# Performance work log

Hardware: AMD Instinct MI355X
Metric: run time of the kernel (lower is better)

The kernel has to match this reference:

```python
import jax, jax.numpy as jnp
import numpy as np

N = 100000   # nodes
E = 1600000  # edges
D_IN, D_H, D_OUT = 128, 128, 64
BN_EPS = 1e-5


def setup_inputs() -> dict:
    key = jax.random.key(0)
    ks = jax.random.split(key, 12)

    def lin_w(k, fan_in, shape):
        s = 1.0 / np.sqrt(fan_in)
        return jax.random.uniform(k, shape, jnp.float32, -s, s)

    return {
        "x": jax.random.normal(ks[0], (N, D_IN), jnp.float32),
        "edge_index": jax.random.randint(ks[1], (2, E), 0, N, dtype=jnp.int64),
        "edge_weight": jax.random.uniform(ks[2], (E,), jnp.float32),
        "W1": lin_w(ks[3], D_IN, (D_IN, D_H)),
        "b1": jnp.zeros((D_H,), jnp.float32),
        "W2": lin_w(ks[4], D_H, (D_H, D_H)),
        "b2": jnp.zeros((D_H,), jnp.float32),
        "W3": lin_w(ks[5], D_H, (D_H, D_OUT)),
        "b3": jnp.zeros((D_OUT,), jnp.float32),
        "gamma1": jnp.ones((D_H,), jnp.float32),
        "beta1": jnp.zeros((D_H,), jnp.float32),
        "gamma2": jnp.ones((D_H,), jnp.float32),
        "beta2": jnp.zeros((D_H,), jnp.float32),
    }


def _gcn_conv(x, src, dst, w, W, b):
    # PyG GCNConv: x' = D^{-1/2} (A + I) D^{-1/2} (x W) + b, self-loop weight 1
    n = x.shape[0]
    h = x @ W                                   # [N, d_out]
    loop = jnp.arange(n, dtype=src.dtype)
    s = jnp.concatenate([src, loop])            # [E+N]
    d = jnp.concatenate([dst, loop])
    ww = jnp.concatenate([w, jnp.ones((n,), w.dtype)])
    deg = jax.ops.segment_sum(ww, d, num_segments=n)          # in-degree at targets
    dinv = jnp.where(deg > 0, jax.lax.rsqrt(deg), 0.0)
    norm = dinv[s] * ww * dinv[d]               # [E+N]
    msg = h[s] * norm[:, None]                  # gather + scale
    out = jax.ops.segment_sum(msg, d, num_segments=n)
    return out + b


def _batch_norm(x, gamma, beta):
    mean = jnp.mean(x, axis=0)
    var = jnp.mean(jnp.square(x - mean), axis=0)  # biased, as BatchNorm uses
    return (x - mean) * jax.lax.rsqrt(var + BN_EPS) * gamma + beta


def reference(x, edge_index, edge_weight, W1, b1, W2, b2, W3, b3,
              gamma1, beta1, gamma2, beta2):
    src, dst = edge_index[0], edge_index[1]
    h = _gcn_conv(x, src, dst, edge_weight, W1, b1)
    h = jax.nn.relu(_batch_norm(h, gamma1, beta1))
    h = _gcn_conv(h, src, dst, edge_weight, W2, b2)
    h = jax.nn.relu(_batch_norm(h, gamma2, beta2))
    return _gcn_conv(h, src, dst, edge_weight, W3, b3)
```

## Files before the change

kernel.cpp:

```cpp
#include <hip/hip_runtime.h>
#include <hip/hip_fp16.h>
#include <cstdint>
#include <cstddef>

#define BN_EPS 1e-5f
#define KB 1024
#define BSH 9

typedef _Float16 half8 __attribute__((ext_vector_type(8)));
typedef float floatx4 __attribute__((ext_vector_type(4)));

__device__ __forceinline__ float loadS(const __half* p) { return __half2float(*p); }
__device__ __forceinline__ float2 load2(const __half* p) {
    return __half22float2(*(const __half2*)p);
}
__device__ __forceinline__ void storeS(float* p, float v) { *p = v; }
__device__ __forceinline__ void storeS(__half* p, float v) { *p = __float2half(v); }
__device__ __forceinline__ void store2(float* p, float a, float b) {
    *(float2*)p = make_float2(a, b);
}
__device__ __forceinline__ void store2(__half* p, float a, float b) {
    *(__half2*)p = __floats2half2_rn(a, b);
}
__device__ __forceinline__ float wn_of(unsigned v) {
    __half_raw hr; hr.x = (unsigned short)(v & 0x7fffu);
    return __half2float((__half)hr);
}

static __device__ __forceinline__ int load_edge(const void* ei, int mode64, long long pos) {
    if (mode64) return (int)((const long long*)ei)[pos];
    return ((const int*)ei)[pos];
}

__device__ __forceinline__ int detect_mode64(const unsigned* eiw) {
    const int lane = (int)threadIdx.x & 63;
    unsigned m = 0;
    for (int i = lane; i < 2048; i += 64) m |= eiw[2 * i + 1];
    return (__ballot(m != 0) == 0ULL) ? 1 : 0;
}

__global__ __launch_bounds__(256) void init_hist_kernel(const void* __restrict__ ei,
                                                        unsigned* __restrict__ tk,
                                                        unsigned* __restrict__ pc, int E, int epb,
                                                        const float* __restrict__ W1,
                                                        const float* __restrict__ W2,
                                                        const float* __restrict__ W3,
                                                        _Float16* __restrict__ WT1,
                                                        _Float16* __restrict__ WT2,
                                                        _Float16* __restrict__ WT3) {
    const int bid = (int)blockIdx.x;
    const int tid = (int)threadIdx.x;
    if (bid < 160) {
        if (bid == 0 && tid < 8) tk[tid] = 0u;
        const int t_ = bid;
        if (t_ < 64) {
            int t = t_ * 256 + tid;
            int n = t / 128, k = t % 128;
            WT1[t] = (_Float16)W1[k * 128 + n];
        } else if (t_ < 128) {
            int t = (t_ - 64) * 256 + tid;
            int n = t / 128, k = t % 128;
            WT2[t] = (_Float16)W2[k * 128 + n];
        } else {
            int t = (t_ - 128) * 256 + tid;
            int n = t / 128, k = t % 128;
            WT3[t] = (_Float16)W3[k * 64 + n];
        }
        return;
    }
    __shared__ unsigned h[256];
    const int k = bid - 160;
    h[tid] = 0;
    __syncthreads();
    const int md = detect_mode64((const unsigned*)ei);
    const int e0 = k * epb;
    const int e1 = min(E, e0 + epb);
    for (int e = e0 + tid; e < e1; e += 256) {
        int d = load_edge(ei, md, (long long)E + e);
        atomicAdd(&h[d >> BSH], 1u);
    }
    __syncthreads();
    pc[k * 256 + tid] = h[tid];
}

__global__ __launch_bounds__(256) void scan_pc_kernel(unsigned* __restrict__ pc,
                                                      int* __restrict__ tb,
                                                      int* __restrict__ bbase,
                                                      float* __restrict__ gsum,
                                                      float* __restrict__ gsq,
                                                      unsigned* __restrict__ tk, int nbuck) {
    __shared__ int red[256];
    __shared__ int lastFlag;
    const int b = (int)blockIdx.x;
    const int tid = (int)threadIdx.x;
    unsigned v[4];
    int vals[4];
    int s = 0;
#pragma unroll
    for (int j = 0; j < 4; ++j) {
        v[j] = pc[(tid * 4 + j) * 256 + b];
        vals[j] = s;
        s += (int)v[j];
    }
    red[tid] = s;
    __syncthreads();
    for (int off = 1; off < 256; off <<= 1) {
        int t = 0;
        if (tid >= off) t = red[tid - off];
        __syncthreads();
        red[tid] += t;
        __syncthreads();
    }
    const int excl = red[tid] - s;
#pragma unroll
    for (int j = 0; j < 4; ++j)
        pc[(tid * 4 + j) * 256 + b] = (unsigned)(excl + vals[j]);
    if (tid == 255)
        __hip_atomic_store(&tb[b], red[255], __ATOMIC_RELEASE, __HIP_MEMORY_SCOPE_AGENT);
    __syncthreads();
    if (tid == 0) {
        unsigned t = __hip_atomic_fetch_add(tk, 1u, __ATOMIC_ACQ_REL, __HIP_MEMORY_SCOPE_AGENT);
        lastFlag = (t == (unsigned)gridDim.x - 1u) ? 1 : 0;
    }
    __syncthreads();
    if (!lastFlag) return;
    const int v2 = (tid < nbuck)
        ? __hip_atomic_load(&tb[tid], __ATOMIC_ACQUIRE, __HIP_MEMORY_SCOPE_AGENT) : 0;
    __syncthreads();
    red[tid] = v2;
    __syncthreads();
    for (int off = 1; off < 256; off <<= 1) {
        int t = 0;
        if (tid >= off) t = red[tid - off];
        __syncthreads();
        red[tid] += t;
        __syncthreads();
    }
    bbase[tid] = red[tid] - v2;
    if (tid < 128) { gsum[tid] = 0.0f; gsq[tid] = 0.0f; }
}

template <int M, bool BN, typename TI>
__device__ __forceinline__ void gemm_body(int gbid, const TI* __restrict__ X,
                                          const _Float16* __restrict__ WTg,
                                          const float* __restrict__ sc,
                                          const float* __restrict__ sh,
                                          __half* __restrict__ Hout, int N,
                                          _Float16* WT ) {
    constexpr int CT = M / 16;
    constexpr int LDK = 136;

    for (int t = threadIdx.x; t < M * 16; t += 256) {
        int n = t / 16, seg = t % 16;
        *(half8*)&WT[n * LDK + seg * 8] = *(const half8*)&WTg[n * 128 + seg * 8];
    }
    __syncthreads();

    const int wave = (int)threadIdx.x >> 6;
    const int lane = (int)threadIdx.x & 63;
    const int qd = lane >> 4;
    const int ln = lane & 15;
    const int tile0 = gbid * 64 + wave * 16;
    int ar = tile0 + ln;
    if (ar >= N) ar = N - 1;

    half8 aF[4];
    const TI* xr = X + (size_t)ar * 128 + qd * 8;
#pragma unroll
    for (int kb = 0; kb < 4; ++kb) {
        float vv[8];
        if constexpr (sizeof(TI) == 4) {
            float4 v0 = *(const float4*)(xr + kb * 32);
            float4 v1 = *(const float4*)(xr + kb * 32 + 4);
            vv[0] = v0.x; vv[1] = v0.y; vv[2] = v0.z; vv[3] = v0.w;
            vv[4] = v1.x; vv[5] = v1.y; vv[6] = v1.z; vv[7] = v1.w;
        } else {
            half8 raw = *(const half8*)(xr + kb * 32);
#pragma unroll
            for (int j = 0; j < 8; ++j) vv[j] = (float)raw[j];
        }
        if (BN) {
            const int kbase = kb * 32 + qd * 8;
#pragma unroll
            for (int j = 0; j < 8; ++j)
                vv[j] = fmaxf(fmaf(vv[j], sc[kbase + j], sh[kbase + j]), 0.0f);
        }
        half8 a;
#pragma unroll
        for (int j = 0; j < 8; ++j) a[j] = (_Float16)vv[j];
        aF[kb] = a;
    }

#pragma unroll
    for (int ct = 0; ct < CT; ++ct) {
        floatx4 acc = {0.0f, 0.0f, 0.0f, 0.0f};
#pragma unroll
        for (int kb = 0; kb < 4; ++kb) {
            half8 b = *(const half8*)&WT[(ct * 16 + ln) * LDK + kb * 32 + qd * 8];
            acc = __builtin_amdgcn_mfma_f32_16x16x32_f16(aF[kb], b, acc, 0, 0, 0);
        }
#pragma unroll
        for (int r = 0; r < 4; ++r) {
            int orow = tile0 + qd * 4 + r;
            if (orow < N) Hout[(size_t)orow * M + ct * 16 + ln] = __float2half(acc[r]);
        }
    }
}

__global__ __launch_bounds__(256) void sort_gemm1_kernel(const void* __restrict__ ei,
                                                         const float* __restrict__ ew,
                                                         const unsigned* __restrict__ pc,
                                                         const int* __restrict__ bbase,
                                                         unsigned long long* __restrict__ sortedE,
                                                         int E, int epb,
                                                         const float* __restrict__ X,
                                                         const _Float16* __restrict__ WT1g,
                                                         __half* __restrict__ Hout, int N) {
    __shared__ _Float16 WT[128 * 136];
    __shared__ unsigned off_s[256];
    if ((int)blockIdx.x >= KB) {
        gemm_body<128, false, float>((int)blockIdx.x - KB, X, WT1g, nullptr, nullptr,
                                     Hout, N, WT);
        return;
    }
    const int k = (int)blockIdx.x;
    const int tid = (int)threadIdx.x;
    off_s[tid] = (unsigned)bbase[tid] + pc[k * 256 + tid];
    __syncthreads();
    const int md = detect_mode64((const unsigned*)ei);
    const int e0 = k * epb;
    const int e1 = min(E, e0 + epb);
    for (int e = e0 + tid; e < e1; e += 256) {
        int d = load_edge(ei, md, (long long)E + e);
        int s = load_edge(ei, md, e);
        float wv = ew[e];
        unsigned slot = atomicAdd(&off_s[d >> BSH], 1u);
        sortedE[slot] = ((unsigned long long)(unsigned)d << 33) |
                        ((unsigned long long)(unsigned)s << 16) |
                        (unsigned long long)(unsigned short)__half_as_ushort(__float2half(wv));
    }
}

__global__ __launch_bounds__(256) void csr_build_kernel(const unsigned long long* __restrict__ sortedE,
                                                        const int* __restrict__ bbase,
                                                        const int* __restrict__ tb,
                                                        float* __restrict__ dinv,
                                                        int* __restrict__ cnt,
                                                        int* __restrict__ row_start,
                                                        unsigned* __restrict__ edata, int N) {
    __shared__ unsigned cs[512];
    __shared__ float ws[512];
    __shared__ float dv[512];
    __shared__ unsigned sc[512];
    __shared__ unsigned cur[512];
    __shared__ int red[256];
    const int b = (int)blockIdx.x;
    const int tid = (int)threadIdx.x;
    const int n0 = b << BSH;
    const int base = bbase[b];
    const int len = tb[b];

    cs[tid] = 0; cs[tid + 256] = 0;
    ws[tid] = 0.0f; ws[tid + 256] = 0.0f;
    cur[tid] = 0; cur[tid + 256] = 0;
    __syncthreads();

    for (int i = tid; i < len; i += 256) {
        unsigned long long p = sortedE[base + i];
        unsigned fine = (unsigned)(p >> 33) - (unsigned)n0;
        atomicAdd(&cs[fine], 1u);
        __half_raw hr; hr.x = (unsigned short)(p & 0xFFFFu);
        atomicAdd(&ws[fine], __half2float((__half)hr));
    }
    __syncthreads();

    const unsigned a0 = cs[2 * tid];
    const unsigned a1 = cs[2 * tid + 1];
    const int s2 = (int)(a0 + a1);
    red[tid] = s2;
    __syncthreads();
    for (int off = 1; off < 256; off <<= 1) {
        int t = 0;
        if (tid >= off) t = red[tid - off];
        __syncthreads();
        red[tid] += t;
        __syncthreads();
    }
    const int excl2 = red[tid] - s2;
    sc[2 * tid] = (unsigned)excl2;
    sc[2 * tid + 1] = (unsigned)(excl2 + (int)a0);

#pragma unroll
    for (int q = 0; q < 2; ++q) {
        const int f = tid + q * 256;
        const int node = n0 + f;
        const float dvv = rsqrtf(1.0f + ws[f]);
        dv[f] = dvv;
        if (node < N) {
            dinv[node] = dvv;
            cnt[node] = (int)cs[f];
            row_start[node] = base + (int)sc[f];
        }
    }
    __syncthreads();

    for (int i = tid; i < len; i += 256) {
        unsigned long long p = sortedE[base + i];
        unsigned fine = (unsigned)(p >> 33) - (unsigned)n0;
        unsigned s = (unsigned)(p >> 16) & 0x1FFFFu;
        __half_raw hr; hr.x = (unsigned short)(p & 0xFFFFu);
        float wnp = __half2float((__half)hr) * dv[fine];
        unsigned r = atomicAdd(&cur[fine], 1u);
        unsigned hb = (unsigned)__half_as_ushort(__float2half(wnp)) & 0x7fffu;
        edata[base + (int)sc[fine] + (int)r] = (s << 15) | hb;
    }
}

template <int D, bool BIAS, typename TY>
__global__ __launch_bounds__(256) void agg_kernel(const __half* __restrict__ H,
                                                  const unsigned* __restrict__ edata,
                                                  const int* __restrict__ row_start,
                                                  const int* __restrict__ cnt,
                                                  const float* __restrict__ dinv,
                                                  const float* __restrict__ bias,
                                                  TY* __restrict__ Y, int N) {
    constexpr int VPT = D / 64;
    const int lane = (int)threadIdx.x & 63;
    const int i = (int)blockIdx.x * 4 + ((int)threadIdx.x >> 6);
    if (i >= N) return;
    const int c0 = lane * VPT;
    const float di = dinv[i];
    const float dii = di * di;

    float acc0, acc1 = 0.0f;
    if constexpr (VPT == 2) {
        float2 h = load2(H + (size_t)i * D + c0);
        acc0 = dii * h.x;
        acc1 = dii * h.y;
    } else {
        acc0 = dii * loadS(H + (size_t)i * D + c0);
    }

    const int base = row_start[i];
    const int n = cnt[i];
    for (int off = 0; off < n; off += 64) {
        const int rem = n - off;
        unsigned ev = 0;
        if (lane < rem) ev = edata[base + off + lane];
        const int mm = min(64, rem);
        for (int j = 0; j < mm; j += 8) {
            const unsigned e0 = __shfl(ev, j),     e1 = __shfl(ev, j + 1);
            const unsigned e2 = __shfl(ev, j + 2), e3 = __shfl(ev, j + 3);
            const unsigned e4 = __shfl(ev, j + 4), e5 = __shfl(ev, j + 5);
            const unsigned e6 = __shfl(ev, j + 6), e7 = __shfl(ev, j + 7);
            const float w0 = dinv[e0 >> 15] * wn_of(e0);
            const float w1 = dinv[e1 >> 15] * wn_of(e1);
            const float w2 = dinv[e2 >> 15] * wn_of(e2);
            const float w3 = dinv[e3 >> 15] * wn_of(e3);
            const float w4 = dinv[e4 >> 15] * wn_of(e4);
            const float w5 = dinv[e5 >> 15] * wn_of(e5);
            const float w6 = dinv[e6 >> 15] * wn_of(e6);
            const float w7 = dinv[e7 >> 15] * wn_of(e7);
            if constexpr (VPT == 2) {
                float2 h0 = load2(H + (size_t)(e0 >> 15) * D + c0);
                float2 h1 = load2(H + (size_t)(e1 >> 15) * D + c0);
                float2 h2 = load2(H + (size_t)(e2 >> 15) * D + c0);
                float2 h3 = load2(H + (size_t)(e3 >> 15) * D + c0);
                float2 h4 = load2(H + (size_t)(e4 >> 15) * D + c0);
                float2 h5 = load2(H + (size_t)(e5 >> 15) * D + c0);
                float2 h6 = load2(H + (size_t)(e6 >> 15) * D + c0);
                float2 h7 = load2(H + (size_t)(e7 >> 15) * D + c0);
                acc0 = fmaf(w0, h0.x, acc0); acc1 = fmaf(w0, h0.y, acc1);
                acc0 = fmaf(w1, h1.x, acc0); acc1 = fmaf(w1, h1.y, acc1);
                acc0 = fmaf(w2, h2.x, acc0); acc1 = fmaf(w2, h2.y, acc1);
                acc0 = fmaf(w3, h3.x, acc0); acc1 = fmaf(w3, h3.y, acc1);
                acc0 = fmaf(w4, h4.x, acc0); acc1 = fmaf(w4, h4.y, acc1);
                acc0 = fmaf(w5, h5.x, acc0); acc1 = fmaf(w5, h5.y, acc1);
                acc0 = fmaf(w6, h6.x, acc0); acc1 = fmaf(w6, h6.y, acc1);
                acc0 = fmaf(w7, h7.x, acc0); acc1 = fmaf(w7, h7.y, acc1);
            } else {
                float h0 = loadS(H + (size_t)(e0 >> 15) * D + c0);
                float h1 = loadS(H + (size_t)(e1 >> 15) * D + c0);
                float h2 = loadS(H + (size_t)(e2 >> 15) * D + c0);
                float h3 = loadS(H + (size_t)(e3 >> 15) * D + c0);
                float h4 = loadS(H + (size_t)(e4 >> 15) * D + c0);
                float h5 = loadS(H + (size_t)(e5 >> 15) * D + c0);
                float h6 = loadS(H + (size_t)(e6 >> 15) * D + c0);
                float h7 = loadS(H + (size_t)(e7 >> 15) * D + c0);
                acc0 = fmaf(w0, h0, acc0);
                acc0 = fmaf(w1, h1, acc0);
                acc0 = fmaf(w2, h2, acc0);
                acc0 = fmaf(w3, h3, acc0);
                acc0 = fmaf(w4, h4, acc0);
                acc0 = fmaf(w5, h5, acc0);
                acc0 = fmaf(w6, h6, acc0);
                acc0 = fmaf(w7, h7, acc0);
            }
        }
    }

    if constexpr (VPT == 2) {
        if (BIAS) { acc0 += bias[c0]; acc1 += bias[c0 + 1]; }
        store2(Y + (size_t)i * D + c0, acc0, acc1);
    } else {
        if (BIAS) acc0 += bias[c0];
        storeS(Y + (size_t)i * D + c0, acc0);
    }
}

template <int M, bool BN, typename TI, bool ZERO>
__global__ __launch_bounds__(256) void gemm_mfma_kernel(const TI* __restrict__ X,
                                                        const _Float16* __restrict__ WTg,
                                                        const float* __restrict__ sc,
                                                        const float* __restrict__ sh,
                                                        __half* __restrict__ Hout, int N,
                                                        float* __restrict__ gsum,
                                                        float* __restrict__ gsq, int GB) {
    __shared__ _Float16 WT[M * 136];
    if (ZERO && (int)blockIdx.x == GB) {
        if (threadIdx.x < 128) { gsum[threadIdx.x] = 0.0f; gsq[threadIdx.x] = 0.0f; }
        return;
    }
    gemm_body<M, BN, TI>(blockIdx.x, X, WTg, sc, sh, Hout, N, WT);
}

__global__ __launch_bounds__(256) void stats_kernel(const __half* __restrict__ Y,
                                                    float* __restrict__ gsum,
                                                    float* __restrict__ gsq,
                                                    unsigned* __restrict__ tk,
                                                    const float* __restrict__ gamma,
                                                    const float* __restrict__ beta,
                                                    float* __restrict__ sc,
                                                    float* __restrict__ sh, int N) {
    __shared__ float ls[256], lq[256];
    __shared__ int lastFlag;
    const int tid = (int)threadIdx.x;
    const int c = tid & 127;
    const int half_ = tid >> 7;
    float s = 0.0f, q = 0.0f;
    for (int row = (int)blockIdx.x * 2 + half_; row < N; row += 512) {
        float v = __half2float(Y[(size_t)row * 128 + c]);
        s += v;
        q = fmaf(v, v, q);
    }
    ls[tid] = s; lq[tid] = q;
    __syncthreads();
    if (tid < 128) {
        atomicAdd(&gsum[c], ls[tid] + ls[tid + 128]);
        atomicAdd(&gsq[c],  lq[tid] + lq[tid + 128]);
    }
    __syncthreads();
    if (tid == 0) {
        unsigned t = __hip_atomic_fetch_add(tk, 1u, __ATOMIC_ACQ_REL, __HIP_MEMORY_SCOPE_AGENT);
        lastFlag = (t == (unsigned)gridDim.x - 1u) ? 1 : 0;
    }
    __syncthreads();
    if (!lastFlag) return;
    if (tid < 128) {
        float gs = __hip_atomic_load(&gsum[tid], __ATOMIC_ACQUIRE, __HIP_MEMORY_SCOPE_AGENT);
        float gq = __hip_atomic_load(&gsq[tid], __ATOMIC_ACQUIRE, __HIP_MEMORY_SCOPE_AGENT);
        float inv_n = 1.0f / (float)N;
        float mean = gs * inv_n;
        float var = gq * inv_n - mean * mean;
        float scale = gamma[tid] * rsqrtf(var + BN_EPS);
        sc[tid] = scale;
        sh[tid] = beta[tid] - mean * scale;
    }
}

extern "C" void kernel_launch(void* const* d_in, const int* in_sizes, int n_in,
                              void* d_out, int out_size, void* d_ws, size_t ws_size,
                              hipStream_t stream) {
    const float* x   = (const float*)d_in[0];
    const void*  ei  = d_in[1];
    const float* ew  = (const float*)d_in[2];
    const float* W1  = (const float*)d_in[3];
    const float* W2  = (const float*)d_in[5];
    const float* W3  = (const float*)d_in[7];
    const float* b3  = (const float*)d_in[8];
    const float* g1  = (const float*)d_in[9];
    const float* be1 = (const float*)d_in[10];
    const float* g2  = (const float*)d_in[11];
    const float* be2 = (const float*)d_in[12];
    float* out = (float*)d_out;

    const int N = in_sizes[0] / 128;
    const int E = in_sizes[2];

    char* w = (char*)d_ws;
    size_t off = 0;
    auto alloc = [&](size_t bytes) -> void* {
        void* p = w + off;
        off += (bytes + 255) & ~(size_t)255;
        return p;
    };
    unsigned* pc     = (unsigned*)alloc((size_t)KB * 256 * 4);
    int*   tb        = (int*)  alloc(256 * 4);
    int*   bbase     = (int*)  alloc(256 * 4);
    unsigned long long* sortedE = (unsigned long long*)alloc((size_t)E * 8);
    float* dinv      = (float*)alloc((size_t)N * 4);
    int*   cnt       = (int*)  alloc((size_t)N * 4);
    int*   row_start = (int*)  alloc((size_t)N * 4);
    unsigned* edata  = (unsigned*)alloc((size_t)E * 4);
    unsigned* tk     = (unsigned*)alloc(256);
    float* gsum      = (float*)alloc(128 * 4);
    float* gsq       = (float*)alloc(128 * 4);
    float* scb       = (float*)alloc(128 * 4);
    float* shb       = (float*)alloc(128 * 4);
    _Float16* WT1    = (_Float16*)alloc(128 * 128 * 2);
    _Float16* WT2    = (_Float16*)alloc(128 * 128 * 2);
    _Float16* WT3    = (_Float16*)alloc(128 * 64 * 2);
    __half* H        = (__half*)alloc((size_t)N * 128 * 2);
    __half* Yh       = (__half*)alloc((size_t)N * 128 * 2);
    (void)ws_size; (void)n_in; (void)out_size;

    const int epb   = (E + KB - 1) / KB;
    const int nbuck = (N + (1 << BSH) - 1) >> BSH;
    const int gb    = (N + 63) / 64;
    const int ab    = (N + 3) / 4;

    init_hist_kernel<<<160 + KB, 256, 0, stream>>>(ei, tk, pc, E, epb,
                                                   W1, W2, W3, WT1, WT2, WT3);
    scan_pc_kernel<<<nbuck, 256, 0, stream>>>(pc, tb, bbase, gsum, gsq, &tk[0], nbuck);
    sort_gemm1_kernel<<<KB + gb, 256, 0, stream>>>(ei, ew, pc, bbase, sortedE, E,
                                                   epb, x, WT1, H, N);
    csr_build_kernel<<<nbuck, 256, 0, stream>>>(sortedE, bbase, tb, dinv, cnt, row_start,
                                                edata, N);

    agg_kernel<128, false, __half><<<ab, 256, 0, stream>>>(H, edata, row_start, cnt, dinv, nullptr, Yh, N);
    stats_kernel<<<256, 256, 0, stream>>>(Yh, gsum, gsq, &tk[1], g1, be1, scb, shb, N);

    gemm_mfma_kernel<128, true, __half, true><<<gb + 1, 256, 0, stream>>>(
        Yh, WT2, scb, shb, H, N, gsum, gsq, gb);
    agg_kernel<128, false, __half><<<ab, 256, 0, stream>>>(H, edata, row_start, cnt, dinv, nullptr, Yh, N);
    stats_kernel<<<256, 256, 0, stream>>>(Yh, gsum, gsq, &tk[2], g2, be2, scb, shb, N);

    gemm_mfma_kernel<64, true, __half, false><<<gb, 256, 0, stream>>>(
        Yh, WT3, scb, shb, H, N, nullptr, nullptr, gb);
    agg_kernel<64, true, float><<<ab, 256, 0, stream>>>(H, edata, row_start, cnt, dinv, b3, out, N);
}
```

Baseline: 497.7 us.

## Store features in 16-column slabs and aggregate per slab for gather locality

```diff
diff --git a/kernel.cpp b/kernel.cpp
--- a/kernel.cpp
+++ b/kernel.cpp
@@ -11,17 +11,7 @@
 typedef float floatx4 __attribute__((ext_vector_type(4)));
 
 __device__ __forceinline__ float loadS(const __half* p) { return __half2float(*p); }
-__device__ __forceinline__ float2 load2(const __half* p) {
-    return __half22float2(*(const __half2*)p);
-}
 __device__ __forceinline__ void storeS(float* p, float v) { *p = v; }
-__device__ __forceinline__ void storeS(__half* p, float v) { *p = __float2half(v); }
-__device__ __forceinline__ void store2(float* p, float a, float b) {
-    *(float2*)p = make_float2(a, b);
-}
-__device__ __forceinline__ void store2(__half* p, float a, float b) {
-    *(__half2*)p = __floats2half2_rn(a, b);
-}
 __device__ __forceinline__ float wn_of(unsigned v) {
     __half_raw hr; hr.x = (unsigned short)(v & 0x7fffu);
     return __half2float((__half)hr);
@@ -51,7 +41,7 @@
     const int bid = (int)blockIdx.x;
     const int tid = (int)threadIdx.x;
     if (bid < 160) {
-        if (bid == 0 && tid < 8) tk[tid] = 0u;
+        if (bid == 0 && tid < 64) tk[tid] = 0u;
         const int t_ = bid;
         if (t_ < 64) {
             int t = t_ * 256 + tid;
@@ -86,8 +76,7 @@
 __global__ __launch_bounds__(256) void scan_pc_kernel(unsigned* __restrict__ pc,
                                                       int* __restrict__ tb,
                                                       int* __restrict__ bbase,
-                                                      float* __restrict__ gsum,
-                                                      float* __restrict__ gsq,
+                                                      float* __restrict__ gz,
                                                       unsigned* __restrict__ tk, int nbuck) {
     __shared__ int red[256];
     __shared__ int lastFlag;
@@ -137,10 +126,10 @@
         __syncthreads();
     }
     bbase[tid] = red[tid] - v2;
-    if (tid < 128) { gsum[tid] = 0.0f; gsq[tid] = 0.0f; }
-}
-
-template <int M, bool BN, typename TI>
+    gz[tid] = 0.0f; gz[tid + 256] = 0.0f;
+}
+
+template <int M, bool BN, typename TI, bool XS>
 __device__ __forceinline__ void gemm_body(int gbid, const TI* __restrict__ X,
                                           const _Float16* __restrict__ WTg,
                                           const float* __restrict__ sc,
@@ -165,19 +154,21 @@
     if (ar >= N) ar = N - 1;
 
     half8 aF[4];
-    const TI* xr = X + (size_t)ar * 128 + qd * 8;
 #pragma unroll
     for (int kb = 0; kb < 4; ++kb) {
         float vv[8];
-        if constexpr (sizeof(TI) == 4) {
+        if constexpr (XS) {
+            const _Float16* xs = (const _Float16*)X;
+            half8 raw = *(const half8*)&xs[((size_t)(kb * 2 + (qd >> 1)) * N + ar) * 16 +
+                                           (qd & 1) * 8];
+#pragma unroll
+            for (int j = 0; j < 8; ++j) vv[j] = (float)raw[j];
+        } else {
+            const float* xr = (const float*)X + (size_t)ar * 128 + qd * 8;
             float4 v0 = *(const float4*)(xr + kb * 32);
             float4 v1 = *(const float4*)(xr + kb * 32 + 4);
             vv[0] = v0.x; vv[1] = v0.y; vv[2] = v0.z; vv[3] = v0.w;
             vv[4] = v1.x; vv[5] = v1.y; vv[6] = v1.z; vv[7] = v1.w;
-        } else {
-            half8 raw = *(const half8*)(xr + kb * 32);
-#pragma unroll
-            for (int j = 0; j < 8; ++j) vv[j] = (float)raw[j];
         }
         if (BN) {
             const int kbase = kb * 32 + qd * 8;
@@ -202,7 +193,8 @@
 #pragma unroll
         for (int r = 0; r < 4; ++r) {
             int orow = tile0 + qd * 4 + r;
-            if (orow < N) Hout[(size_t)orow * M + ct * 16 + ln] = __float2half(acc[r]);
+            if (orow < N)
+                Hout[((size_t)ct * N + orow) * 16 + ln] = __float2half(acc[r]);
         }
     }
 }
@@ -219,8 +211,8 @@
     __shared__ _Float16 WT[128 * 136];
     __shared__ unsigned off_s[256];
     if ((int)blockIdx.x >= KB) {
-        gemm_body<128, false, float>((int)blockIdx.x - KB, X, WT1g, nullptr, nullptr,
-                                     Hout, N, WT);
+        gemm_body<128, false, float, false>((int)blockIdx.x - KB, X, WT1g, nullptr, nullptr,
+                                            Hout, N, WT);
         return;
     }
     const int k = (int)blockIdx.x;
@@ -317,111 +309,77 @@
 }
 
 template <int D, bool BIAS, typename TY>
-__global__ __launch_bounds__(256) void agg_kernel(const __half* __restrict__ H,
-                                                  const unsigned* __restrict__ edata,
-                                                  const int* __restrict__ row_start,
-                                                  const int* __restrict__ cnt,
-                                                  const float* __restrict__ dinv,
-                                                  const float* __restrict__ bias,
-                                                  TY* __restrict__ Y, int N) {
-    constexpr int VPT = D / 64;
-    const int lane = (int)threadIdx.x & 63;
-    const int i = (int)blockIdx.x * 4 + ((int)threadIdx.x >> 6);
-    if (i >= N) return;
-    const int c0 = lane * VPT;
-    const float di = dinv[i];
-    const float dii = di * di;
-
-    float acc0, acc1 = 0.0f;
-    if constexpr (VPT == 2) {
-        float2 h = load2(H + (size_t)i * D + c0);
-        acc0 = dii * h.x;
-        acc1 = dii * h.y;
-    } else {
-        acc0 = dii * loadS(H + (size_t)i * D + c0);
-    }
-
-    const int base = row_start[i];
-    const int n = cnt[i];
-    for (int off = 0; off < n; off += 64) {
-        const int rem = n - off;
-        unsigned ev = 0;
-        if (lane < rem) ev = edata[base + off + lane];
-        const int mm = min(64, rem);
-        for (int j = 0; j < mm; j += 8) {
-            const unsigned e0 = __shfl(ev, j),     e1 = __shfl(ev, j + 1);
-            const unsigned e2 = __shfl(ev, j + 2), e3 = __shfl(ev, j + 3);
-            const unsigned e4 = __shfl(ev, j + 4), e5 = __shfl(ev, j + 5);
-            const unsigned e6 = __shfl(ev, j + 6), e7 = __shfl(ev, j + 7);
-            const float w0 = dinv[e0 >> 15] * wn_of(e0);
-            const float w1 = dinv[e1 >> 15] * wn_of(e1);
-            const float w2 = dinv[e2 >> 15] * wn_of(e2);
-            const float w3 = dinv[e3 >> 15] * wn_of(e3);
-            const float w4 = dinv[e4 >> 15] * wn_of(e4);
-            const float w5 = dinv[e5 >> 15] * wn_of(e5);
-            const float w6 = dinv[e6 >> 15] * wn_of(e6);
-            const float w7 = dinv[e7 >> 15] * wn_of(e7);
-            if constexpr (VPT == 2) {
-                float2 h0 = load2(H + (size_t)(e0 >> 15) * D + c0);
-                float2 h1 = load2(H + (size_t)(e1 >> 15) * D + c0);
-                float2 h2 = load2(H + (size_t)(e2 >> 15) * D + c0);
-                float2 h3 = load2(H + (size_t)(e3 >> 15) * D + c0);
-                float2 h4 = load2(H + (size_t)(e4 >> 15) * D + c0);
-                float2 h5 = load2(H + (size_t)(e5 >> 15) * D + c0);
-                float2 h6 = load2(H + (size_t)(e6 >> 15) * D + c0);
-                float2 h7 = load2(H + (size_t)(e7 >> 15) * D + c0);
-                acc0 = fmaf(w0, h0.x, acc0); acc1 = fmaf(w0, h0.y, acc1);
-                acc0 = fmaf(w1, h1.x, acc0); acc1 = fmaf(w1, h1.y, acc1);
-                acc0 = fmaf(w2, h2.x, acc0); acc1 = fmaf(w2, h2.y, acc1);
-                acc0 = fmaf(w3, h3.x, acc0); acc1 = fmaf(w3, h3.y, acc1);
-                acc0 = fmaf(w4, h4.x, acc0); acc1 = fmaf(w4, h4.y, acc1);
-                acc0 = fmaf(w5, h5.x, acc0); acc1 = fmaf(w5, h5.y, acc1);
-                acc0 = fmaf(w6, h6.x, acc0); acc1 = fmaf(w6, h6.y, acc1);
-                acc0 = fmaf(w7, h7.x, acc0); acc1 = fmaf(w7, h7.y, acc1);
+__global__ __launch_bounds__(256) void agg_slice_kernel(const _Float16* __restrict__ Hs,
+                                                        const unsigned* __restrict__ edata,
+                                                        const int* __restrict__ row_start,
+                                                        const int* __restrict__ cnt,
+                                                        const float* __restrict__ dinv,
+                                                        const float* __restrict__ bias,
+                                                        TY* __restrict__ Y, int N) {
+    constexpr int NSL = D / 16;
+    const int bid = (int)blockIdx.x;
+    const int s = bid & (NSL - 1);
+    const int g = bid / NSL;
+    const int tid = (int)threadIdx.x;
+    const int wv = tid >> 6;
+    const int lane = tid & 63;
+    const int q = lane >> 4;
+    const int lq = lane & 15;
+    const _Float16* __restrict__ slab = Hs + (size_t)s * N * 16;
+
+#pragma unroll 1
+    for (int rep = 0; rep < 8; ++rep) {
+        const int i = g * 32 + wv * 8 + rep;
+        if (i >= N) break;
+        const float di = dinv[i];
+        float acc = (q == 0) ? di * di * (float)slab[(size_t)i * 16 + lq] : 0.0f;
+        const int base = row_start[i];
+        const int n = cnt[i];
+        for (int off = 0; off < n; off += 64) {
+            const int rem = n - off;
+            unsigned ev = 0;
+            if (lane < rem) ev = edata[base + off + lane];
+            const int mm = min(64, rem);
+            for (int j = 0; j < mm; j += 16) {
+                const unsigned e0 = __shfl(ev, (j + q) & 63);
+                const unsigned e1 = __shfl(ev, (j + 4 + q) & 63);
+                const unsigned e2 = __shfl(ev, (j + 8 + q) & 63);
+                const unsigned e3 = __shfl(ev, (j + 12 + q) & 63);
+                const float w0 = dinv[e0 >> 15] * wn_of(e0);
+                const float w1 = dinv[e1 >> 15] * wn_of(e1);
+                const float w2 = dinv[e2 >> 15] * wn_of(e2);
+                const float w3 = dinv[e3 >> 15] * wn_of(e3);
+                const float h0 = (float)slab[(size_t)(e0 >> 15) * 16 + lq];
+                const float h1 = (float)slab[(size_t)(e1 >> 15) * 16 + lq];
+                const float h2 = (float)slab[(size_t)(e2 >> 15) * 16 + lq];
+                const float h3 = (float)slab[(size_t)(e3 >> 15) * 16 + lq];
+                acc = fmaf(w0, h0, acc);
+                acc = fmaf(w1, h1, acc);
+                acc = fmaf(w2, h2, acc);
+                acc = fmaf(w3, h3, acc);
+            }
+        }
+        acc += __shfl_xor(acc, 16);
+        acc += __shfl_xor(acc, 32);
+        if (q == 0) {
+            if constexpr (BIAS) acc += bias[s * 16 + lq];
+            if constexpr (sizeof(TY) == 2) {
+                ((__half*)Y)[((size_t)s * N + i) * 16 + lq] = __float2half(acc);
             } else {
-                float h0 = loadS(H + (size_t)(e0 >> 15) * D + c0);
-                float h1 = loadS(H + (size_t)(e1 >> 15) * D + c0);
-                float h2 = loadS(H + (size_t)(e2 >> 15) * D + c0);
-                float h3 = loadS(H + (size_t)(e3 >> 15) * D + c0);
-                float h4 = loadS(H + (size_t)(e4 >> 15) * D + c0);
-                float h5 = loadS(H + (size_t)(e5 >> 15) * D + c0);
-                float h6 = loadS(H + (size_t)(e6 >> 15) * D + c0);
-                float h7 = loadS(H + (size_t)(e7 >> 15) * D + c0);
-                acc0 = fmaf(w0, h0, acc0);
-                acc0 = fmaf(w1, h1, acc0);
-                acc0 = fmaf(w2, h2, acc0);
-                acc0 = fmaf(w3, h3, acc0);
-                acc0 = fmaf(w4, h4, acc0);
-                acc0 = fmaf(w5, h5, acc0);
-                acc0 = fmaf(w6, h6, acc0);
-                acc0 = fmaf(w7, h7, acc0);
+                ((float*)Y)[(size_t)i * D + s * 16 + lq] = acc;
             }
         }
     }
-
-    if constexpr (VPT == 2) {
-        if (BIAS) { acc0 += bias[c0]; acc1 += bias[c0 + 1]; }
-        store2(Y + (size_t)i * D + c0, acc0, acc1);
-    } else {
-        if (BIAS) acc0 += bias[c0];
-        storeS(Y + (size_t)i * D + c0, acc0);
-    }
-}
-
-template <int M, bool BN, typename TI, bool ZERO>
-__global__ __launch_bounds__(256) void gemm_mfma_kernel(const TI* __restrict__ X,
+}
+
+template <int M>
+__global__ __launch_bounds__(256) void gemm_mfma_kernel(const __half* __restrict__ X,
                                                         const _Float16* __restrict__ WTg,
                                                         const float* __restrict__ sc,
                                                         const float* __restrict__ sh,
-                                                        __half* __restrict__ Hout, int N,
-                                                        float* __restrict__ gsum,
-                                                        float* __restrict__ gsq, int GB) {
+                                                        __half* __restrict__ Hout, int N) {
     __shared__ _Float16 WT[M * 136];
-    if (ZERO && (int)blockIdx.x == GB) {
-        if (threadIdx.x < 128) { gsum[threadIdx.x] = 0.0f; gsq[threadIdx.x] = 0.0f; }
-        return;
-    }
-    gemm_body<M, BN, TI>(blockIdx.x, X, WTg, sc, sh, Hout, N, WT);
+    gemm_body<M, true, __half, true>(blockIdx.x, X, WTg, sc, sh, Hout, N, WT);
 }
 
 __global__ __launch_bounds__(256) void stats_kernel(const __half* __restrict__ Y,
@@ -437,9 +395,10 @@
     const int tid = (int)threadIdx.x;
     const int c = tid & 127;
     const int half_ = tid >> 7;
+    const __half* __restrict__ Yc = Y + (size_t)(c >> 4) * N * 16 + (c & 15);
     float s = 0.0f, q = 0.0f;
     for (int row = (int)blockIdx.x * 2 + half_; row < N; row += 512) {
-        float v = __half2float(Y[(size_t)row * 128 + c]);
+        float v = __half2float(Yc[(size_t)row * 16]);
         s += v;
         q = fmaf(v, v, q);
     }
@@ -503,8 +462,7 @@
     int*   row_start = (int*)  alloc((size_t)N * 4);
     unsigned* edata  = (unsigned*)alloc((size_t)E * 4);
     unsigned* tk     = (unsigned*)alloc(256);
-    float* gsum      = (float*)alloc(128 * 4);
-    float* gsq       = (float*)alloc(128 * 4);
+    float* gz        = (float*)alloc(512 * 4);
     float* scb       = (float*)alloc(128 * 4);
     float* shb       = (float*)alloc(128 * 4);
     _Float16* WT1    = (_Float16*)alloc(128 * 128 * 2);
@@ -514,28 +472,34 @@
     __half* Yh       = (__half*)alloc((size_t)N * 128 * 2);
     (void)ws_size; (void)n_in; (void)out_size;
 
+    float* gsumA = gz,        *gsqA = gz + 128;
+    float* gsumB = gz + 256,  *gsqB = gz + 384;
+
     const int epb   = (E + KB - 1) / KB;
     const int nbuck = (N + (1 << BSH) - 1) >> BSH;
     const int gb    = (N + 63) / 64;
-    const int ab    = (N + 3) / 4;
+    const int ngrp  = (N + 31) / 32;
+    const int ag8   = ngrp * 8;
+    const int ag4   = ngrp * 4;
 
     init_hist_kernel<<<160 + KB, 256, 0, stream>>>(ei, tk, pc, E, epb,
                                                    W1, W2, W3, WT1, WT2, WT3);
-    scan_pc_kernel<<<nbuck, 256, 0, stream>>>(pc, tb, bbase, gsum, gsq, &tk[0], nbuck);
+    scan_pc_kernel<<<nbuck, 256, 0, stream>>>(pc, tb, bbase, gz, &tk[0], nbuck);
     sort_gemm1_kernel<<<KB + gb, 256, 0, stream>>>(ei, ew, pc, bbase, sortedE, E,
                                                    epb, x, WT1, H, N);
     csr_build_kernel<<<nbuck, 256, 0, stream>>>(sortedE, bbase, tb, dinv, cnt, row_start,
                                                 edata, N);
 
-    agg_kernel<128, false, __half><<<ab, 256, 0, stream>>>(H, edata, row_start, cnt, dinv, nullptr, Yh, N);
-    stats_kernel<<<256, 256, 0, stream>>>(Yh, gsum, gsq, &tk[1], g1, be1, scb, shb, N);
-
-    gemm_mfma_kernel<128, true, __half, true><<<gb + 1, 256, 0, stream>>>(
-        Yh, WT2, scb, shb, H, N, gsum, gsq, gb);
-    agg_kernel<128, false, __half><<<ab, 256, 0, stream>>>(H, edata, row_start, cnt, dinv, nullptr, Yh, N);
-    stats_kernel<<<256, 256, 0, stream>>>(Yh, gsum, gsq, &tk[2], g2, be2, scb, shb, N);
-
-    gemm_mfma_kernel<64, true, __half, false><<<gb, 256, 0, stream>>>(
-        Yh, WT3, scb, shb, H, N, nullptr, nullptr, gb);
-    agg_kernel<64, true, float><<<ab, 256, 0, stream>>>(H, edata, row_start, cnt, dinv, b3, out, N);
-}
+    agg_slice_kernel<128, false, __half><<<ag8, 256, 0, stream>>>(
+        (const _Float16*)H, edata, row_start, cnt, dinv, nullptr, Yh, N);
+    stats_kernel<<<256, 256, 0, stream>>>(Yh, gsumA, gsqA, &tk[1], g1, be1, scb, shb, N);
+
+    gemm_mfma_kernel<128><<<gb, 256, 0, stream>>>(Yh, WT2, scb, shb, H, N);
+    agg_slice_kernel<128, false, __half><<<ag8, 256, 0, stream>>>(
+        (const _Float16*)H, edata, row_start, cnt, dinv, nullptr, Yh, N);
+    stats_kernel<<<256, 256, 0, stream>>>(Yh, gsumB, gsqB, &tk[2], g2, be2, scb, shb, N);
+
+    gemm_mfma_kernel<64><<<gb, 256, 0, stream>>>(Yh, WT3, scb, shb, H, N);
+    agg_slice_kernel<64, true, float><<<ag4, 256, 0, stream>>>(
+        (const _Float16*)H, edata, row_start, cnt, dinv, b3, out, N);
+}
```

New measurement: 869.4 us. 1.75x slower.
